# Kernel optimization log

Measured on AMD Instinct MI355X. Metric: run time of the kernel, lower is better.

The kernel has to match this reference:

```python
import jax, jax.numpy as jnp
import numpy as np

ATTR_LEN = [2, 4, 4, 2, 6]
CUM = np.concatenate(([0], np.cumsum(ATTR_LEN)))  # [0,2,6,10,12,18]
B, S, D, V = 4096, 200, 64, 100000


def setup_inputs() -> dict:
    key = jax.random.key(0)
    ks = jax.random.split(key, 10)
    x = jax.random.randint(ks[0], (B, S), 0, V)
    # one-hot labels per attribute, concatenated -> [B, 18]
    y_parts = []
    for i, al in enumerate(ATTR_LEN):
        lab = jax.random.randint(jax.random.fold_in(ks[1], i), (B,), 0, al)
        y_parts.append(jax.nn.one_hot(lab, al, dtype=jnp.float32))
    y = jnp.concatenate(y_parts, axis=1)
    emb_table = jax.random.normal(ks[2], (V, D), jnp.float32) * 0.02
    emb_table = emb_table.at[0].set(0.0)  # padding_idx=0
    att_w = jax.random.normal(ks[3], (5, D), jnp.float32) * 0.1
    att_b = jax.random.normal(ks[4], (5,), jnp.float32) * 0.1
    W0 = jax.random.normal(ks[5], (ATTR_LEN[0], D), jnp.float32) * 0.1
    W1 = jax.random.normal(ks[6], (ATTR_LEN[1], D), jnp.float32) * 0.1
    W2 = jax.random.normal(ks[7], (ATTR_LEN[2], D), jnp.float32) * 0.1
    W3 = jax.random.normal(ks[8], (ATTR_LEN[3], D), jnp.float32) * 0.1
    W4 = jax.random.normal(ks[9], (ATTR_LEN[4], D), jnp.float32) * 0.1
    return {"x": x, "y": y, "emb_table": emb_table, "att_w": att_w,
            "att_b": att_b, "W0": W0, "W1": W1, "W2": W2, "W3": W3, "W4": W4}


def reference(x, y, emb_table, att_w, att_b, W0, W1, W2, W3, W4):
    embed = emb_table[x]  # [B, S, D] gather (padding row is zero)
    # 5 per-attribute additive tanh-attention heads, batched over k.
    # Softmax over seq axis is independent per head, so stacking is exact.
    att_u = jnp.tanh(jnp.einsum('bsd,kd->bsk', embed, att_w) + att_b)  # [B,S,5]
    score = jax.nn.softmax(att_u, axis=1)                              # [B,S,5]
    user_rep = jnp.einsum('bsd,bsk->bkd', embed, score)                # [B,5,D]
    Ws = [W0, W1, W2, W3, W4]
    # per-task bias-free linear heads, concatenated -> [B, 18]
    W_user = jnp.concatenate([user_rep[:, i] @ Ws[i].T for i in range(5)], axis=1)
    logits = []
    loss = jnp.float32(0.0)
    for i in range(5):
        Wc = W_user[:, CUM[i]:CUM[i + 1]]
        yc = y[:, CUM[i]:CUM[i + 1]]
        # partial_training=False -> ob = ones -> all rows kept;
        # obj = exp(sum(W*y)) / sum_j exp(W_j)  ==  softmax picked at label
        logp = jax.nn.log_softmax(Wc, axis=1)
        loss = loss + (-jnp.sum(logp * yc) / Wc.shape[0])
        logits.append(jax.nn.softmax(Wc, axis=1))
    logit = jnp.concatenate(logits, axis=1)  # [B, 18]
    return logit, loss
```

## Files before the change

### kernel.cpp

```cpp
#include <hip/hip_runtime.h>
#include <math.h>

#define Bsz 4096
#define Ssz 200
#define Dsz 64
#define NK  5
#define NT  512
#define ROWH 72

typedef _Float16 half_t;
typedef _Float16 h2 __attribute__((ext_vector_type(2)));

__device__ inline h2 shfl_xor_h2(h2 v, int m) {
    int iv = __builtin_bit_cast(int, v);
    iv = __shfl_xor(iv, m);
    return __builtin_bit_cast(h2, iv);
}

__device__ inline float fdot2(h2 a, h2 b, float c) {
#if __has_builtin(__builtin_amdgcn_fdot2)
    return __builtin_amdgcn_fdot2(a, b, c, false);
#else
    return c + (float)a.x * (float)b.x + (float)a.y * (float)b.y;
#endif
}

__global__ void loss_reduce_kernel(const float* __restrict__ pb,
                                   float* __restrict__ loss) {
    const int l = threadIdx.x;
    float s = 0.f;
    for (int i = l; i < Bsz; i += 64) s += pb[i];
#pragma unroll
    for (int m = 32; m >= 1; m >>= 1) s += __shfl_xor(s, m);
    if (l == 0) *loss = s * (1.0f / Bsz);
}

__global__ __launch_bounds__(NT, 8) void tan_kernel(
    const int* __restrict__ x, const float* __restrict__ y,
    const float* __restrict__ emb_table,
    const float* __restrict__ att_w, const float* __restrict__ att_b,
    const float* __restrict__ W0, const float* __restrict__ W1,
    const float* __restrict__ W2, const float* __restrict__ W3,
    const float* __restrict__ W4,
    float* __restrict__ out_logit, float* __restrict__ loss_ws)
{
    __shared__ alignas(16) half_t embh[Ssz * ROWH];
    __shared__ alignas(16) float  att[NK][Ssz];
    __shared__ alignas(16) h2     awh[NK * 32];
    __shared__ alignas(16) half_t urph[8][NK][Dsz];
    __shared__ alignas(16) float  ur[NK][Dsz];
    __shared__ alignas(16) int    xs[Ssz];
    __shared__ float wu[18];

    const int b   = blockIdx.x;
    const int tid = threadIdx.x;
    const int w   = tid >> 6;
    const int l   = tid & 63;

    if (tid < Ssz) xs[tid] = x[b * Ssz + tid];
    if (tid >= 256 && tid < 256 + NK * 32) {
        const int t = tid - 256;
        awh[t] = (h2){(half_t)att_w[2 * t], (half_t)att_w[2 * t + 1]};
    }
    __syncthreads();

    {
        float4 v[7];
#pragma unroll
        for (int p = 0; p < 7; ++p) {
            int i = tid + NT * p;
            if (i > Ssz * 16 - 1) i = Ssz * 16 - 1;
            const int s = i >> 4, c = i & 15;
            v[p] = ((const float4*)(emb_table + (size_t)xs[s] * Dsz))[c];
        }
#pragma unroll
        for (int p = 0; p < 7; ++p) {
            const int i = tid + NT * p;
            if (p < 6 || i < Ssz * 16) {
                const int s = i >> 4, c = i & 15;
                h2 a  = (h2){(half_t)v[p].x, (half_t)v[p].y};
                h2 b2 = (h2){(half_t)v[p].z, (half_t)v[p].w};
                uint2 u = { __builtin_bit_cast(unsigned, a),
                            __builtin_bit_cast(unsigned, b2) };
                *(uint2*)(embh + s * ROWH + c * 4) = u;
            }
        }
    }
    __syncthreads();

    if (tid < 2 * Ssz) {
        const int s = tid >> 1, h = tid & 1;
        union { uint4 q[4]; h2 hh[16]; } ue;
        const uint4* rp = (const uint4*)(embh + s * ROWH + h * 32);
#pragma unroll
        for (int i = 0; i < 4; ++i) ue.q[i] = rp[i];
        float acc[NK];
#pragma unroll 1
        for (int k = 0; k < NK; ++k) {
            union { uint4 q[4]; h2 hh[16]; } ua;
            const uint4* ap = (const uint4*)(awh + k * 32 + h * 16);
#pragma unroll
            for (int i = 0; i < 4; ++i) ua.q[i] = ap[i];
            float a = 0.f;
#pragma unroll
            for (int i = 0; i < 16; ++i) a = fdot2(ue.hh[i], ua.hh[i], a);
            acc[k] = a;
        }
#pragma unroll
        for (int k = 0; k < NK; ++k) acc[k] += __shfl_xor(acc[k], 1);
        if (h == 0) {
#pragma unroll
            for (int k = 0; k < NK; ++k) att[k][s] = tanhf(acc[k] + att_b[k]);
        }
    }
    __syncthreads();

    if (w < NK) {
        const int k = w;
        float vals[4];
        float mx = -1e30f;
#pragma unroll
        for (int j = 0; j < 4; ++j) {
            int s = l + 64 * j;
            vals[j] = (s < Ssz) ? att[k][s] : -1e30f;
            mx = fmaxf(mx, vals[j]);
        }
#pragma unroll
        for (int m = 32; m >= 1; m >>= 1) mx = fmaxf(mx, __shfl_xor(mx, m));
        float sum = 0.f;
#pragma unroll
        for (int j = 0; j < 4; ++j) {
            vals[j] = __expf(vals[j] - mx);
            sum += vals[j];
        }
#pragma unroll
        for (int m = 32; m >= 1; m >>= 1) sum += __shfl_xor(sum, m);
        float inv = 1.0f / sum;
#pragma unroll
        for (int j = 0; j < 4; ++j) {
            int s = l + 64 * j;
            if (s < Ssz) att[k][s] = vals[j] * inv;
        }
    }
    __syncthreads();

    {
        const int c = tid & 7;
        const int j = tid >> 3;
        h2 acc[NK][4];
#pragma unroll
        for (int k = 0; k < NK; ++k)
#pragma unroll
            for (int i = 0; i < 4; ++i) acc[k][i] = (h2){(half_t)0, (half_t)0};
#pragma unroll
        for (int t = 0; t < 4; ++t) {
            const int s = j + 64 * t;
            if (s < Ssz) {
                union { uint4 q; h2 hh[4]; } u;
                u.q = *(const uint4*)(embh + s * ROWH + c * 8);
#pragma unroll
                for (int k = 0; k < NK; ++k) {
                    half_t f = (half_t)att[k][s];
                    h2 sc = (h2){f, f};
#pragma unroll
                    for (int i = 0; i < 4; ++i) acc[k][i] += u.hh[i] * sc;
                }
            }
        }
#pragma unroll
        for (int k = 0; k < NK; ++k)
#pragma unroll
            for (int i = 0; i < 4; ++i) {
                acc[k][i] += shfl_xor_h2(acc[k][i], 8);
                acc[k][i] += shfl_xor_h2(acc[k][i], 16);
                acc[k][i] += shfl_xor_h2(acc[k][i], 32);
            }
        if (l < 8) {
#pragma unroll
            for (int k = 0; k < NK; ++k) {
                union { h2 a[4]; uint4 q; } uu;
#pragma unroll
                for (int i = 0; i < 4; ++i) uu.a[i] = acc[k][i];
                *(uint4*)(&urph[w][k][l * 8]) = uu.q;
            }
        }
    }
    __syncthreads();

    if (tid < NK * Dsz) {
        const int k = tid >> 6, d = tid & 63;
        float ssum = 0.f;
#pragma unroll
        for (int jj = 0; jj < 8; ++jj) ssum += (float)urph[jj][k][d];
        ur[k][d] = ssum;
    }
    __syncthreads();

    for (int j = w; j < 18; j += 8) {
        const float* Wp; int g, c0;
        if      (j < 2)  { g = 0; c0 = 0;  Wp = W0; }
        else if (j < 6)  { g = 1; c0 = 2;  Wp = W1; }
        else if (j < 10) { g = 2; c0 = 6;  Wp = W2; }
        else if (j < 12) { g = 3; c0 = 10; Wp = W3; }
        else             { g = 4; c0 = 12; Wp = W4; }
        float p = ur[g][l] * Wp[(j - c0) * Dsz + l];
#pragma unroll
        for (int m = 32; m >= 1; m >>= 1) p += __shfl_xor(p, m);
        if (l == 0) wu[j] = p;
    }
    __syncthreads();

    if (w == 0) {
        float lossb = 0.f;
        if (l < NK) {
            const int LEN[5] = {2, 4, 4, 2, 6};
            const int C0[5]  = {0, 2, 6, 10, 12};
            const int g = l, c0 = C0[g], len = LEN[g];
            float* op = out_logit + (size_t)b * 18;
            const float* yp = y + (size_t)b * 18;
            float mx = -1e30f;
            for (int j = 0; j < len; ++j) mx = fmaxf(mx, wu[c0 + j]);
            float sum = 0.f;
            for (int j = 0; j < len; ++j) sum += __expf(wu[c0 + j] - mx);
            float inv = 1.0f / sum;
            float lse = mx + __logf(sum);
            for (int j = 0; j < len; ++j) {
                op[c0 + j] = __expf(wu[c0 + j] - mx) * inv;
                lossb += (lse - wu[c0 + j]) * yp[c0 + j];
            }
        }
#pragma unroll
        for (int m = 1; m <= 4; m <<= 1) lossb += __shfl_xor(lossb, m);
        if (l == 0) loss_ws[b] = lossb;
    }
}

extern "C" void kernel_launch(void* const* d_in, const int* in_sizes, int n_in,
                              void* d_out, int out_size, void* d_ws, size_t ws_size,
                              hipStream_t stream) {
    const int*   x   = (const int*)d_in[0];
    const float* y   = (const float*)d_in[1];
    const float* emb = (const float*)d_in[2];
    const float* aw  = (const float*)d_in[3];
    const float* ab  = (const float*)d_in[4];
    const float* W0  = (const float*)d_in[5];
    const float* W1  = (const float*)d_in[6];
    const float* W2  = (const float*)d_in[7];
    const float* W3  = (const float*)d_in[8];
    const float* W4  = (const float*)d_in[9];
    float* out  = (float*)d_out;
    float* loss = out + (size_t)Bsz * 18;
    float* pb   = (float*)d_ws;

    tan_kernel<<<Bsz, NT, 0, stream>>>(x, y, emb, aw, ab,
                                       W0, W1, W2, W3, W4, out, pb);
    loss_reduce_kernel<<<1, 64, 0, stream>>>(pb, loss);
}
```

Baseline: 164.0 us.

## Fuse loss reduction via atomics, drop index staging, use fast tanh and packed converts

```diff
diff --git a/kernel.cpp b/kernel.cpp
--- a/kernel.cpp
+++ b/kernel.cpp
@@ -25,14 +25,14 @@
 #endif
 }
 
-__global__ void loss_reduce_kernel(const float* __restrict__ pb,
-                                   float* __restrict__ loss) {
-    const int l = threadIdx.x;
-    float s = 0.f;
-    for (int i = l; i < Bsz; i += 64) s += pb[i];
-#pragma unroll
-    for (int m = 32; m >= 1; m >>= 1) s += __shfl_xor(s, m);
-    if (l == 0) *loss = s * (1.0f / Bsz);
+__device__ inline float fast_tanh(float x) {
+    float e = __expf(-2.0f * fabsf(x));
+    float r = (1.0f - e) / (1.0f + e);
+    return copysignf(r, x);
+}
+
+__global__ void zero_loss_kernel(float* loss) {
+    if (threadIdx.x == 0) *loss = 0.0f;
 }
 
 __global__ __launch_bounds__(NT, 8) void tan_kernel(
@@ -42,14 +42,12 @@
     const float* __restrict__ W0, const float* __restrict__ W1,
     const float* __restrict__ W2, const float* __restrict__ W3,
     const float* __restrict__ W4,
-    float* __restrict__ out_logit, float* __restrict__ loss_ws)
+    float* __restrict__ out_logit, float* __restrict__ loss_out)
 {
     __shared__ alignas(16) half_t embh[Ssz * ROWH];
     __shared__ alignas(16) float  att[NK][Ssz];
     __shared__ alignas(16) h2     awh[NK * 32];
     __shared__ alignas(16) half_t urph[8][NK][Dsz];
-    __shared__ alignas(16) float  ur[NK][Dsz];
-    __shared__ alignas(16) int    xs[Ssz];
     __shared__ float wu[18];
 
     const int b   = blockIdx.x;
@@ -57,31 +55,29 @@
     const int w   = tid >> 6;
     const int l   = tid & 63;
 
-    if (tid < Ssz) xs[tid] = x[b * Ssz + tid];
-    if (tid >= 256 && tid < 256 + NK * 32) {
-        const int t = tid - 256;
-        awh[t] = (h2){(half_t)att_w[2 * t], (half_t)att_w[2 * t + 1]};
-    }
-    __syncthreads();
+    if (tid < NK * 32)
+        awh[tid] = (h2){(half_t)att_w[2 * tid], (half_t)att_w[2 * tid + 1]};
 
     {
+        const int* xb = x + b * Ssz;
         float4 v[7];
 #pragma unroll
         for (int p = 0; p < 7; ++p) {
             int i = tid + NT * p;
             if (i > Ssz * 16 - 1) i = Ssz * 16 - 1;
             const int s = i >> 4, c = i & 15;
-            v[p] = ((const float4*)(emb_table + (size_t)xs[s] * Dsz))[c];
+            const int xi = xb[s];
+            v[p] = ((const float4*)(emb_table + (size_t)xi * Dsz))[c];
         }
 #pragma unroll
         for (int p = 0; p < 7; ++p) {
             const int i = tid + NT * p;
             if (p < 6 || i < Ssz * 16) {
                 const int s = i >> 4, c = i & 15;
-                h2 a  = (h2){(half_t)v[p].x, (half_t)v[p].y};
-                h2 b2 = (h2){(half_t)v[p].z, (half_t)v[p].w};
-                uint2 u = { __builtin_bit_cast(unsigned, a),
-                            __builtin_bit_cast(unsigned, b2) };
+                h2 lo = __builtin_bit_cast(h2, __builtin_amdgcn_cvt_pkrtz(v[p].x, v[p].y));
+                h2 hi = __builtin_bit_cast(h2, __builtin_amdgcn_cvt_pkrtz(v[p].z, v[p].w));
+                uint2 u = { __builtin_bit_cast(unsigned, lo),
+                            __builtin_bit_cast(unsigned, hi) };
                 *(uint2*)(embh + s * ROWH + c * 4) = u;
             }
         }
@@ -101,16 +97,21 @@
             const uint4* ap = (const uint4*)(awh + k * 32 + h * 16);
 #pragma unroll
             for (int i = 0; i < 4; ++i) ua.q[i] = ap[i];
-            float a = 0.f;
-#pragma unroll
-            for (int i = 0; i < 16; ++i) a = fdot2(ue.hh[i], ua.hh[i], a);
-            acc[k] = a;
+            float a0 = 0.f, a1 = 0.f, a2 = 0.f, a3 = 0.f;
+#pragma unroll
+            for (int i = 0; i < 4; ++i) {
+                a0 = fdot2(ue.hh[4 * i + 0], ua.hh[4 * i + 0], a0);
+                a1 = fdot2(ue.hh[4 * i + 1], ua.hh[4 * i + 1], a1);
+                a2 = fdot2(ue.hh[4 * i + 2], ua.hh[4 * i + 2], a2);
+                a3 = fdot2(ue.hh[4 * i + 3], ua.hh[4 * i + 3], a3);
+            }
+            acc[k] = (a0 + a1) + (a2 + a3);
         }
 #pragma unroll
         for (int k = 0; k < NK; ++k) acc[k] += __shfl_xor(acc[k], 1);
         if (h == 0) {
 #pragma unroll
-            for (int k = 0; k < NK; ++k) att[k][s] = tanhf(acc[k] + att_b[k]);
+            for (int k = 0; k < NK; ++k) att[k][s] = fast_tanh(acc[k] + att_b[k]);
         }
     }
     __syncthreads();
@@ -153,17 +154,22 @@
 #pragma unroll
             for (int i = 0; i < 4; ++i) acc[k][i] = (h2){(half_t)0, (half_t)0};
 #pragma unroll
-        for (int t = 0; t < 4; ++t) {
-            const int s = j + 64 * t;
-            if (s < Ssz) {
-                union { uint4 q; h2 hh[4]; } u;
-                u.q = *(const uint4*)(embh + s * ROWH + c * 8);
+        for (int t = 0; t < 2; ++t) {
+            const int s0 = 2 * j + 128 * t;
+            if (s0 < Ssz) {
+                union { uint4 q; h2 hh[4]; } u0, u1;
+                u0.q = *(const uint4*)(embh + s0 * ROWH + c * 8);
+                u1.q = *(const uint4*)(embh + (s0 + 1) * ROWH + c * 8);
 #pragma unroll
                 for (int k = 0; k < NK; ++k) {
-                    half_t f = (half_t)att[k][s];
-                    h2 sc = (h2){f, f};
-#pragma unroll
-                    for (int i = 0; i < 4; ++i) acc[k][i] += u.hh[i] * sc;
+                    float2 scf = *(const float2*)(&att[k][s0]);
+                    half_t f0 = (half_t)scf.x, f1 = (half_t)scf.y;
+                    h2 sc0 = (h2){f0, f0}, sc1 = (h2){f1, f1};
+#pragma unroll
+                    for (int i = 0; i < 4; ++i) {
+                        acc[k][i] += u0.hh[i] * sc0;
+                        acc[k][i] += u1.hh[i] * sc1;
+                    }
                 }
             }
         }
@@ -184,15 +190,6 @@
                 *(uint4*)(&urph[w][k][l * 8]) = uu.q;
             }
         }
-    }
-    __syncthreads();
-
-    if (tid < NK * Dsz) {
-        const int k = tid >> 6, d = tid & 63;
-        float ssum = 0.f;
-#pragma unroll
-        for (int jj = 0; jj < 8; ++jj) ssum += (float)urph[jj][k][d];
-        ur[k][d] = ssum;
     }
     __syncthreads();
 
@@ -203,7 +200,10 @@
         else if (j < 10) { g = 2; c0 = 6;  Wp = W2; }
         else if (j < 12) { g = 3; c0 = 10; Wp = W3; }
         else             { g = 4; c0 = 12; Wp = W4; }
-        float p = ur[g][l] * Wp[(j - c0) * Dsz + l];
+        float urv = 0.f;
+#pragma unroll
+        for (int jj = 0; jj < 8; ++jj) urv += (float)urph[jj][g][l];
+        float p = urv * Wp[(j - c0) * Dsz + l];
 #pragma unroll
         for (int m = 32; m >= 1; m >>= 1) p += __shfl_xor(p, m);
         if (l == 0) wu[j] = p;
@@ -231,7 +231,7 @@
         }
 #pragma unroll
         for (int m = 1; m <= 4; m <<= 1) lossb += __shfl_xor(lossb, m);
-        if (l == 0) loss_ws[b] = lossb;
+        if (l == 0) atomicAdd(loss_out, lossb * (1.0f / Bsz));
     }
 }
 
@@ -250,9 +250,8 @@
     const float* W4  = (const float*)d_in[9];
     float* out  = (float*)d_out;
     float* loss = out + (size_t)Bsz * 18;
-    float* pb   = (float*)d_ws;
-
+
+    zero_loss_kernel<<<1, 64, 0, stream>>>(loss);
     tan_kernel<<<Bsz, NT, 0, stream>>>(x, y, emb, aw, ab,
-                                       W0, W1, W2, W3, W4, out, pb);
-    loss_reduce_kernel<<<1, 64, 0, stream>>>(pb, loss);
-}
+                                       W0, W1, W2, W3, W4, out, loss);
+}
```

Measured after the change: 157.2 us. 1.04x faster.

## Use packed conversions, fast tanh, fuse user-rep reduction, atomic loss accumulation

Applied to the files above, without the earlier changes.

```diff
diff --git a/kernel.cpp b/kernel.cpp
--- a/kernel.cpp
+++ b/kernel.cpp
@@ -17,6 +17,10 @@
     return __builtin_bit_cast(h2, iv);
 }
 
+__device__ inline h2 pk(float a, float b) {
+    return __builtin_bit_cast(h2, __builtin_amdgcn_cvt_pkrtz(a, b));
+}
+
 __device__ inline float fdot2(h2 a, h2 b, float c) {
 #if __has_builtin(__builtin_amdgcn_fdot2)
     return __builtin_amdgcn_fdot2(a, b, c, false);
@@ -25,14 +29,14 @@
 #endif
 }
 
-__global__ void loss_reduce_kernel(const float* __restrict__ pb,
-                                   float* __restrict__ loss) {
-    const int l = threadIdx.x;
-    float s = 0.f;
-    for (int i = l; i < Bsz; i += 64) s += pb[i];
-#pragma unroll
-    for (int m = 32; m >= 1; m >>= 1) s += __shfl_xor(s, m);
-    if (l == 0) *loss = s * (1.0f / Bsz);
+__device__ inline float fast_tanh(float x) {
+    float e = __expf(-2.0f * fabsf(x));
+    float r = (1.0f - e) / (1.0f + e);
+    return copysignf(r, x);
+}
+
+__global__ void zero_loss_kernel(float* loss) {
+    if (threadIdx.x == 0) *loss = 0.0f;
 }
 
 __global__ __launch_bounds__(NT, 8) void tan_kernel(
@@ -42,13 +46,12 @@
     const float* __restrict__ W0, const float* __restrict__ W1,
     const float* __restrict__ W2, const float* __restrict__ W3,
     const float* __restrict__ W4,
-    float* __restrict__ out_logit, float* __restrict__ loss_ws)
+    float* __restrict__ out_logit, float* __restrict__ loss_out)
 {
     __shared__ alignas(16) half_t embh[Ssz * ROWH];
     __shared__ alignas(16) float  att[NK][Ssz];
     __shared__ alignas(16) h2     awh[NK * 32];
     __shared__ alignas(16) half_t urph[8][NK][Dsz];
-    __shared__ alignas(16) float  ur[NK][Dsz];
     __shared__ alignas(16) int    xs[Ssz];
     __shared__ float wu[18];
 
@@ -78,10 +81,10 @@
             const int i = tid + NT * p;
             if (p < 6 || i < Ssz * 16) {
                 const int s = i >> 4, c = i & 15;
-                h2 a  = (h2){(half_t)v[p].x, (half_t)v[p].y};
-                h2 b2 = (h2){(half_t)v[p].z, (half_t)v[p].w};
-                uint2 u = { __builtin_bit_cast(unsigned, a),
-                            __builtin_bit_cast(unsigned, b2) };
+                h2 lo = pk(v[p].x, v[p].y);
+                h2 hi = pk(v[p].z, v[p].w);
+                uint2 u = { __builtin_bit_cast(unsigned, lo),
+                            __builtin_bit_cast(unsigned, hi) };
                 *(uint2*)(embh + s * ROWH + c * 4) = u;
             }
         }
@@ -110,7 +113,7 @@
         for (int k = 0; k < NK; ++k) acc[k] += __shfl_xor(acc[k], 1);
         if (h == 0) {
 #pragma unroll
-            for (int k = 0; k < NK; ++k) att[k][s] = tanhf(acc[k] + att_b[k]);
+            for (int k = 0; k < NK; ++k) att[k][s] = fast_tanh(acc[k] + att_b[k]);
         }
     }
     __syncthreads();
@@ -184,15 +187,6 @@
                 *(uint4*)(&urph[w][k][l * 8]) = uu.q;
             }
         }
-    }
-    __syncthreads();
-
-    if (tid < NK * Dsz) {
-        const int k = tid >> 6, d = tid & 63;
-        float ssum = 0.f;
-#pragma unroll
-        for (int jj = 0; jj < 8; ++jj) ssum += (float)urph[jj][k][d];
-        ur[k][d] = ssum;
     }
     __syncthreads();
 
@@ -203,7 +197,10 @@
         else if (j < 10) { g = 2; c0 = 6;  Wp = W2; }
         else if (j < 12) { g = 3; c0 = 10; Wp = W3; }
         else             { g = 4; c0 = 12; Wp = W4; }
-        float p = ur[g][l] * Wp[(j - c0) * Dsz + l];
+        float urv = 0.f;
+#pragma unroll
+        for (int jj = 0; jj < 8; ++jj) urv += (float)urph[jj][g][l];
+        float p = urv * Wp[(j - c0) * Dsz + l];
 #pragma unroll
         for (int m = 32; m >= 1; m >>= 1) p += __shfl_xor(p, m);
         if (l == 0) wu[j] = p;
@@ -231,7 +228,7 @@
         }
 #pragma unroll
         for (int m = 1; m <= 4; m <<= 1) lossb += __shfl_xor(lossb, m);
-        if (l == 0) loss_ws[b] = lossb;
+        if (l == 0) atomicAdd(loss_out, lossb * (1.0f / Bsz));
     }
 }
 
@@ -250,9 +247,8 @@
     const float* W4  = (const float*)d_in[9];
     float* out  = (float*)d_out;
     float* loss = out + (size_t)Bsz * 18;
-    float* pb   = (float*)d_ws;
-
+
+    zero_loss_kernel<<<1, 64, 0, stream>>>(loss);
     tan_kernel<<<Bsz, NT, 0, stream>>>(x, y, emb, aw, ab,
-                                       W0, W1, W2, W3, W4, out, pb);
-    loss_reduce_kernel<<<1, 64, 0, stream>>>(pb, loss);
-}
+                                       W0, W1, W2, W3, W4, out, loss);
+}
```

Result: faster. 154.8 us (-5.7%).
